# Performance work log

Hardware: AMD Instinct MI355X
Metric: run time of the kernel (lower is better)

Reference implementation:

```python
import jax, jax.numpy as jnp
import numpy as np

HIDDEN = 2048
N_HEADS = 32
N_KV_HEADS = 8
HEAD_DIM = HIDDEN // N_HEADS  # 64
N_REP = N_HEADS // N_KV_HEADS  # 4
ROPE_THETA = 10000.0


def setup_inputs() -> dict:
    key = jax.random.key(0)
    ks = jax.random.split(key, 5)
    b, s = 2, 2048
    x = jax.random.normal(ks[0], (b, s, HIDDEN), dtype=jnp.float32)
    position_ids = jnp.arange(b * s, dtype=jnp.int32).reshape(b, s)
    sc = 1.0 / np.sqrt(HIDDEN)
    Wq = jax.random.normal(ks[1], (HIDDEN, HIDDEN), dtype=jnp.float32) * sc
    Wk = jax.random.normal(ks[2], (HIDDEN, N_KV_HEADS * HEAD_DIM), dtype=jnp.float32) * sc
    Wv = jax.random.normal(ks[3], (HIDDEN, N_KV_HEADS * HEAD_DIM), dtype=jnp.float32) * sc
    Wo = jax.random.normal(ks[4], (HIDDEN, HIDDEN), dtype=jnp.float32) * sc
    return {"input_ids": x, "Wq": Wq, "Wk": Wk, "Wv": Wv, "Wo": Wo,
            "position_ids": position_ids}


def _rope_cos_sin(position_ids, dtype):
    # inv_freq: [head_dim/2]
    inv_freq = 1.0 / (ROPE_THETA ** (jnp.arange(0, HEAD_DIM, 2, dtype=jnp.float32) / HEAD_DIM))
    freqs = position_ids.astype(jnp.float32)[..., None] * inv_freq  # [b, s, d/2]
    emb = jnp.concatenate([freqs, freqs], axis=-1)  # [b, s, d]
    return emb.astype(dtype), None  # placeholder, replaced below


def _rotate_half(x):
    x1, x2 = jnp.split(x, 2, axis=-1)
    return jnp.concatenate([-x2, x1], axis=-1)


def reference(input_ids, Wq, Wk, Wv, Wo, position_ids):
    b, s, _ = input_ids.shape
    q = (input_ids @ Wq).reshape(b, s, N_HEADS, HEAD_DIM).transpose(0, 2, 1, 3)      # [b,H,s,d]
    k = (input_ids @ Wk).reshape(b, s, N_KV_HEADS, HEAD_DIM).transpose(0, 2, 1, 3)   # [b,Hkv,s,d]
    v = (input_ids @ Wv).reshape(b, s, N_KV_HEADS, HEAD_DIM).transpose(0, 2, 1, 3)

    # RoPE
    inv_freq = 1.0 / (ROPE_THETA ** (jnp.arange(0, HEAD_DIM, 2, dtype=jnp.float32) / HEAD_DIM))
    freqs = position_ids.astype(jnp.float32)[..., None] * inv_freq  # [b,s,d/2]
    emb = jnp.concatenate([freqs, freqs], axis=-1)                   # [b,s,d]
    cos = jnp.cos(emb).astype(input_ids.dtype)[:, None, :, :]        # [b,1,s,d]
    sin = jnp.sin(emb).astype(input_ids.dtype)[:, None, :, :]
    q = q * cos + _rotate_half(q) * sin
    k = k * cos + _rotate_half(k) * sin

    # repeat_kv: [b,Hkv,s,d] -> [b,H,s,d]
    k = jnp.repeat(k, N_REP, axis=1)
    v = jnp.repeat(v, N_REP, axis=1)

    # causal SDPA
    scale = 1.0 / np.sqrt(HEAD_DIM)
    scores = jnp.einsum('bhqd,bhkd->bhqk', q, k) * scale
    causal = jnp.tril(jnp.ones((s, s), dtype=bool))
    scores = jnp.where(causal, scores, jnp.finfo(scores.dtype).min)
    attn = jax.nn.softmax(scores, axis=-1)
    out = jnp.einsum('bhqk,bhkd->bhqd', attn, v)                     # [b,H,s,d]
    out = out.transpose(0, 2, 1, 3).reshape(b, s, HIDDEN)
    return out @ Wo
```

## Files before the change

### kernel.cpp

```cpp
#include <hip/hip_runtime.h>
#include <hip/hip_bf16.h>

#define HIDDEN 2048
#define NHEADS 32
#define NKVH   8
#define HD     64
#define BATCH  2
#define SEQ    2048
#define ROWS   (BATCH * SEQ)
#define NQKV   3072
#define KCOL   2048
#define VCOL   2560

typedef __bf16 bf16x8 __attribute__((ext_vector_type(8)));
typedef float  f32x4  __attribute__((ext_vector_type(4)));

__device__ __forceinline__ void gl2lds16(const void* g, void* l) {
  __builtin_amdgcn_global_load_lds(
      (const __attribute__((address_space(1))) void*)g,
      (__attribute__((address_space(3))) void*)l, 16, 0, 0);
}

__global__ void convert_bf16(const float* __restrict__ src, __bf16* __restrict__ dst,
                             int n8) {
  int i = blockIdx.x * blockDim.x + threadIdx.x;
  if (i >= n8) return;
  const float4* s = (const float4*)(src + (size_t)i * 8);
  float4 a = s[0], b = s[1];
  bf16x8 o;
  o[0] = (__bf16)a.x; o[1] = (__bf16)a.y; o[2] = (__bf16)a.z; o[3] = (__bf16)a.w;
  o[4] = (__bf16)b.x; o[5] = (__bf16)b.y; o[6] = (__bf16)b.z; o[7] = (__bf16)b.w;
  *(bf16x8*)(dst + (size_t)i * 8) = o;
}

__global__ void wtrans(const float* __restrict__ Wq, const float* __restrict__ Wk,
                       const float* __restrict__ Wv, const float* __restrict__ Wo,
                       __bf16* __restrict__ dst) {
  __shared__ __bf16 tile[32][33];
  int n0 = blockIdx.x * 32, k0 = blockIdx.y * 32;
  int tx = threadIdx.x, ty = threadIdx.y;
  const float* src;
  int N, c0;
  if (n0 < 2048)      { src = Wq; N = 2048; c0 = n0; }
  else if (n0 < 2560) { src = Wk; N = 512;  c0 = n0 - 2048; }
  else if (n0 < 3072) { src = Wv; N = 512;  c0 = n0 - 2560; }
  else                { src = Wo; N = 2048; c0 = n0 - 3072; }
#pragma unroll
  for (int i = 0; i < 32; i += 8)
    tile[ty + i][tx] = (__bf16)src[(size_t)(k0 + ty + i) * N + (c0 + tx)];
  __syncthreads();
#pragma unroll
  for (int i = 0; i < 32; i += 8)
    dst[(size_t)(n0 + ty + i) * HIDDEN + (k0 + tx)] = tile[tx][ty + i];
}

__global__ void vtrans(const __bf16* __restrict__ QKV, __bf16* __restrict__ Vt) {
  __shared__ __bf16 tile[64][65];
  int s0 = blockIdx.x * 64, bh = blockIdx.y;
  int b = bh >> 3, hk = bh & 7;
  int tx = threadIdx.x, ty = threadIdx.y;
#pragma unroll
  for (int i = 0; i < 16; ++i) {
    int r = ty * 16 + i;
    tile[r][tx] = QKV[(size_t)(b * SEQ + s0 + r) * NQKV + VCOL + hk * HD + tx];
  }
  __syncthreads();
#pragma unroll
  for (int i = 0; i < 16; ++i) {
    int d = ty * 16 + i;
    Vt[((size_t)bh * HD + d) * SEQ + s0 + tx] = tile[tx][d];
  }
}

template <typename OutT, bool ROPE>
__launch_bounds__(256, 2)
__global__ void gemm_bt(const __bf16* __restrict__ A, const __bf16* __restrict__ Bt,
                        OutT* __restrict__ C, int M, int N, int K,
                        const int* __restrict__ pos_ids) {
  __shared__ __bf16 As[128 * 32];
  __shared__ __bf16 Bs[128 * 32];
  int bn = blockIdx.x, bm = blockIdx.y;
  int t = threadIdx.x;
  int wave = t >> 6, lane = t & 63, l16 = lane & 15, quad = lane >> 4;
  int wm = (wave >> 1) * 64, wn = (wave & 1) * 64;

  f32x4 acc[4][4] = {};

  int arow = t >> 2;
  int ac   = (t & 3) * 8;
  const __bf16* Ag = A  + (size_t)(bm * 128 + arow) * K + ac;
  const __bf16* Bg = Bt + (size_t)(bn * 128 + arow) * K + ac;
  __bf16* AsW0 = As + wave * 512;
  __bf16* AsW1 = As + 2048 + wave * 512;
  __bf16* BsW0 = Bs + wave * 512;
  __bf16* BsW1 = Bs + 2048 + wave * 512;

  for (int k0 = 0; k0 < K; k0 += 32) {
    __syncthreads();
    gl2lds16(Ag + k0, AsW0);
    gl2lds16(Ag + (size_t)64 * K + k0, AsW1);
    gl2lds16(Bg + k0, BsW0);
    gl2lds16(Bg + (size_t)64 * K + k0, BsW1);
    __syncthreads();

    bf16x8 af[4], bfr[4];
#pragma unroll
    for (int i = 0; i < 4; ++i) {
      af[i]  = *(const bf16x8*)(&As[(wm + i * 16 + l16) * 32 + quad * 8]);
      bfr[i] = *(const bf16x8*)(&Bs[(wn + i * 16 + l16) * 32 + quad * 8]);
    }
#pragma unroll
    for (int i = 0; i < 4; ++i)
#pragma unroll
      for (int j = 0; j < 4; ++j)
        acc[i][j] = __builtin_amdgcn_mfma_f32_16x16x32_bf16(af[i], bfr[j], acc[i][j], 0, 0, 0);
  }

  if (ROPE) {
    int headidx = bn * 2 + (wn >> 6);
    if (headidx < 40) {
      float invrev0 = __expf(-(float)l16 * 0.28782313662425574f) * 0.15915494309189535f;
      float invrev1 = __expf(-(float)(l16 + 16) * 0.28782313662425574f) * 0.15915494309189535f;
#pragma unroll
      for (int i = 0; i < 4; ++i)
#pragma unroll
        for (int r = 0; r < 4; ++r) {
          int gr = bm * 128 + wm + i * 16 + quad * 4 + r;
          float pos = (float)pos_ids[gr];
          float rv0 = pos * invrev0; rv0 -= floorf(rv0);
          float rv1 = pos * invrev1; rv1 -= floorf(rv1);
          float a0 = rv0 * 6.283185307179586f, a1 = rv1 * 6.283185307179586f;
          float s0 = __sinf(a0), c0 = __cosf(a0);
          float s1 = __sinf(a1), c1 = __cosf(a1);
          float x0 = acc[i][0][r], x2 = acc[i][2][r];
          acc[i][0][r] = x0 * c0 - x2 * s0;
          acc[i][2][r] = x2 * c0 + x0 * s0;
          float x1 = acc[i][1][r], x3 = acc[i][3][r];
          acc[i][1][r] = x1 * c1 - x3 * s1;
          acc[i][3][r] = x3 * c1 + x1 * s1;
        }
    }
  }

#pragma unroll
  for (int i = 0; i < 4; ++i)
#pragma unroll
    for (int j = 0; j < 4; ++j)
#pragma unroll
      for (int r = 0; r < 4; ++r)
        C[(size_t)(bm * 128 + wm + i * 16 + quad * 4 + r) * N +
          (bn * 128 + wn + j * 16 + l16)] = (OutT)acc[i][j][r];
}

#define PSTRP 72
__launch_bounds__(256, 3)
__global__ void flash_attn(const __bf16* __restrict__ QKV, const __bf16* __restrict__ Vt,
                           __bf16* __restrict__ O) {
  int qt = 31 - (blockIdx.x >> 1);
  int h2 = blockIdx.x & 1;
  int hk = blockIdx.y, b = blockIdx.z;
  int t = threadIdx.x;
  int wave = t >> 6, lane = t & 63, l16 = lane & 15, quad = lane >> 4;
  int hh = h2 * 2 + (wave >> 1);
  int h  = hk * 4 + hh;
  int qs = wave & 1;

  __shared__ __bf16 Ks[2][2][64 * 32];
  __shared__ __bf16 Vs[2][2][64 * 32];
  __shared__ __bf16 Ps[4][32 * PSTRP];
  __bf16* PsW = Ps[wave];

  const __bf16* Kbase = QKV + (size_t)(b * SEQ) * NQKV + KCOL + hk * HD;
  const __bf16* VtB   = Vt + (size_t)(b * NKVH + hk) * HD * SEQ;

  int kr = wave * 16 + (lane >> 2);
  int kc = (lane & 3) * 8;
  int vd = wave * 16 + (lane >> 2);
  int vc = (lane & 3) * 8;

  bf16x8 qfrag[2][2];
#pragma unroll
  for (int qi = 0; qi < 2; ++qi) {
    const __bf16* qp = QKV + (size_t)(b * SEQ + qt * 64 + qs * 32 + qi * 16 + l16) * NQKV
                     + h * HD + quad * 8;
    bf16x8 q0 = *(const bf16x8*)qp;
    bf16x8 q1 = *(const bf16x8*)(qp + 32);
#pragma unroll
    for (int e = 0; e < 8; ++e) {
      qfrag[qi][0][e] = (__bf16)((float)q0[e] * 0.125f);
      qfrag[qi][1][e] = (__bf16)((float)q1[e] * 0.125f);
    }
  }

  float lsum[2][4];
  f32x4 oacc[2][4];
#pragma unroll
  for (int qi = 0; qi < 2; ++qi) {
#pragma unroll
    for (int r = 0; r < 4; ++r) lsum[qi][r] = 0.f;
#pragma unroll
    for (int nt = 0; nt < 4; ++nt) oacc[qi][nt] = (f32x4){0.f, 0.f, 0.f, 0.f};
  }

  {
    const __bf16* kp = Kbase + (size_t)kr * NQKV + kc;
    gl2lds16(kp,      &Ks[0][0][wave * 512]);
    gl2lds16(kp + 32, &Ks[0][1][wave * 512]);
    const __bf16* vp = VtB + (size_t)vd * SEQ + vc;
    gl2lds16(vp,      &Vs[0][0][wave * 512]);
    gl2lds16(vp + 32, &Vs[0][1][wave * 512]);
  }

  for (int kt = 0; kt <= qt; ++kt) {
    int buf = kt & 1;
    __syncthreads();
    if (kt < qt) {
      const __bf16* kp = Kbase + (size_t)((kt + 1) * 64 + kr) * NQKV + kc;
      gl2lds16(kp,      &Ks[buf ^ 1][0][wave * 512]);
      gl2lds16(kp + 32, &Ks[buf ^ 1][1][wave * 512]);
      const __bf16* vp = VtB + (size_t)vd * SEQ + (kt + 1) * 64 + vc;
      gl2lds16(vp,      &Vs[buf ^ 1][0][wave * 512]);
      gl2lds16(vp + 32, &Vs[buf ^ 1][1][wave * 512]);
    }

    f32x4 sacc[2][4];
#pragma unroll
    for (int qi = 0; qi < 2; ++qi)
#pragma unroll
      for (int nt = 0; nt < 4; ++nt) sacc[qi][nt] = (f32x4){0.f, 0.f, 0.f, 0.f};
#pragma unroll
    for (int ks = 0; ks < 2; ++ks)
#pragma unroll
      for (int nt = 0; nt < 4; ++nt) {
        bf16x8 kf = *(const bf16x8*)(&Ks[buf][ks][(nt * 16 + l16) * 32 + quad * 8]);
#pragma unroll
        for (int qi = 0; qi < 2; ++qi)
          sacc[qi][nt] = __builtin_amdgcn_mfma_f32_16x16x32_bf16(qfrag[qi][ks], kf, sacc[qi][nt], 0, 0, 0);
      }

    float pv[2][4][4];
    if (kt == qt) {
#pragma unroll
      for (int qi = 0; qi < 2; ++qi)
#pragma unroll
        for (int nt = 0; nt < 4; ++nt)
#pragma unroll
          for (int r = 0; r < 4; ++r) {
            int kg = nt * 16 + l16;
            int qg = qs * 32 + qi * 16 + quad * 4 + r;
            pv[qi][nt][r] = __expf((kg > qg) ? -1e30f : sacc[qi][nt][r]);
          }
    } else {
#pragma unroll
      for (int qi = 0; qi < 2; ++qi)
#pragma unroll
        for (int nt = 0; nt < 4; ++nt)
#pragma unroll
          for (int r = 0; r < 4; ++r)
            pv[qi][nt][r] = __expf(sacc[qi][nt][r]);
    }
#pragma unroll
    for (int qi = 0; qi < 2; ++qi)
#pragma unroll
      for (int r = 0; r < 4; ++r)
        lsum[qi][r] += (pv[qi][0][r] + pv[qi][1][r]) + (pv[qi][2][r] + pv[qi][3][r]);

#pragma unroll
    for (int qi = 0; qi < 2; ++qi)
#pragma unroll
      for (int nt = 0; nt < 4; ++nt)
#pragma unroll
        for (int r = 0; r < 4; ++r)
          PsW[(qi * 16 + quad * 4 + r) * PSTRP + nt * 16 + l16] = (__bf16)pv[qi][nt][r];

#pragma unroll
    for (int ks = 0; ks < 2; ++ks) {
      bf16x8 pf[2], vf[4];
#pragma unroll
      for (int qi = 0; qi < 2; ++qi)
        pf[qi] = *(const bf16x8*)(&PsW[(qi * 16 + l16) * PSTRP + ks * 32 + quad * 8]);
#pragma unroll
      for (int nt = 0; nt < 4; ++nt)
        vf[nt] = *(const bf16x8*)(&Vs[buf][ks][(nt * 16 + l16) * 32 + quad * 8]);
#pragma unroll
      for (int qi = 0; qi < 2; ++qi)
#pragma unroll
        for (int nt = 0; nt < 4; ++nt)
          oacc[qi][nt] = __builtin_amdgcn_mfma_f32_16x16x32_bf16(pf[qi], vf[nt], oacc[qi][nt], 0, 0, 0);
    }
  }

#pragma unroll
  for (int qi = 0; qi < 2; ++qi)
#pragma unroll
    for (int r = 0; r < 4; ++r) {
      float l = lsum[qi][r];
#pragma unroll
      for (int off = 1; off < 16; off <<= 1) l += __shfl_xor(l, off);
      float inv = 1.0f / l;
#pragma unroll
      for (int nt = 0; nt < 4; ++nt) {
        float o = oacc[qi][nt][r] * inv;
        O[(size_t)(b * SEQ + qt * 64 + qs * 32 + qi * 16 + quad * 4 + r) * HIDDEN +
          h * HD + nt * 16 + l16] = (__bf16)o;
      }
    }
}

extern "C" void kernel_launch(void* const* d_in, const int* in_sizes, int n_in,
                              void* d_out, int out_size, void* d_ws, size_t ws_size,
                              hipStream_t stream) {
  const float* x  = (const float*)d_in[0];
  const float* Wq = (const float*)d_in[1];
  const float* Wk = (const float*)d_in[2];
  const float* Wv = (const float*)d_in[3];
  const float* Wo = (const float*)d_in[4];
  const int* pos  = (const int*)d_in[5];

  __bf16* Wqkvt = (__bf16*)d_ws;
  __bf16* Wot   = Wqkvt + (size_t)NQKV * HIDDEN;
  __bf16* Xb    = Wot + (size_t)HIDDEN * HIDDEN;
  __bf16* QKV   = Xb + (size_t)ROWS * HIDDEN;
  __bf16* Oat   = QKV + (size_t)ROWS * NQKV;
  __bf16* Vt    = Xb;

  wtrans<<<dim3(160, 64), dim3(32, 8), 0, stream>>>(Wq, Wk, Wv, Wo, Wqkvt);
  convert_bf16<<<(ROWS * HIDDEN / 8 + 255) / 256, 256, 0, stream>>>(x, Xb, ROWS * HIDDEN / 8);

  gemm_bt<__bf16, true><<<dim3(NQKV / 128, ROWS / 128), 256, 0, stream>>>(
      Xb, Wqkvt, QKV, ROWS, NQKV, HIDDEN, pos);

  vtrans<<<dim3(SEQ / 64, BATCH * NKVH), dim3(64, 4), 0, stream>>>(QKV, Vt);

  flash_attn<<<dim3(64, NKVH, BATCH), 256, 0, stream>>>(QKV, Vt, Oat);

  gemm_bt<float, false><<<dim3(HIDDEN / 128, ROWS / 128), 256, 0, stream>>>(
      Oat, Wot, (float*)d_out, ROWS, HIDDEN, HIDDEN, nullptr);
}
```

Before: 324.6 us.

## Fuse V transpose into QKV GEMM, pair causal tiles, keep P in registers

The QKV GEMM epilogue now writes V straight into the transposed Vt layout, so the separate vtrans kernel is gone. Flash attention computes S transposed (K as the A operand), which lets the exponentiated probabilities feed the PV MFMA directly from registers through 16x16x16 bf16 MFMAs. This removes the LDS round trip for P. Each block handles a pair of query tiles (p and 31-p) to balance causal work across a grid half the size. The trade-offs are a V re-layout through registers into LDS and extra MFMA instructions at K=16.

Result: faster. 287.7 us (-11.4%).

```diff
diff --git a/kernel.cpp b/kernel.cpp
--- a/kernel.cpp
+++ b/kernel.cpp
@@ -13,12 +13,33 @@
 #define VCOL   2560
 
 typedef __bf16 bf16x8 __attribute__((ext_vector_type(8)));
+typedef __bf16 bf16x4 __attribute__((ext_vector_type(4)));
 typedef float  f32x4  __attribute__((ext_vector_type(4)));
+typedef short  s16x4  __attribute__((ext_vector_type(4)));
+typedef short  s16x8  __attribute__((ext_vector_type(8)));
 
 __device__ __forceinline__ void gl2lds16(const void* g, void* l) {
   __builtin_amdgcn_global_load_lds(
       (const __attribute__((address_space(1))) void*)g,
       (__attribute__((address_space(3))) void*)l, 16, 0, 0);
+}
+
+__device__ __forceinline__ short f2bs(float f) {
+  __bf16 h = (__bf16)f;
+  return __builtin_bit_cast(short, h);
+}
+
+__device__ __forceinline__ f32x4 mfma16(s16x4 a, s16x4 b, f32x4 c) {
+#if __has_builtin(__builtin_amdgcn_mfma_f32_16x16x16bf16_1k)
+  return __builtin_amdgcn_mfma_f32_16x16x16bf16_1k(a, b, c, 0, 0, 0);
+#else
+  s16x8 z = {0,0,0,0,0,0,0,0};
+  s16x8 a8 = __builtin_shufflevector(a, (s16x4){0,0,0,0}, 0,1,2,3,4,5,6,7);
+  s16x8 b8 = __builtin_shufflevector(b, (s16x4){0,0,0,0}, 0,1,2,3,4,5,6,7);
+  a8[4]=0;a8[5]=0;a8[6]=0;a8[7]=0; b8[4]=0;b8[5]=0;b8[6]=0;b8[7]=0;
+  return __builtin_amdgcn_mfma_f32_16x16x32_bf16(
+      __builtin_bit_cast(bf16x8, a8), __builtin_bit_cast(bf16x8, b8), c, 0, 0, 0);
+#endif
 }
 
 __global__ void convert_bf16(const float* __restrict__ src, __bf16* __restrict__ dst,
@@ -54,29 +75,11 @@
     dst[(size_t)(n0 + ty + i) * HIDDEN + (k0 + tx)] = tile[tx][ty + i];
 }
 
-__global__ void vtrans(const __bf16* __restrict__ QKV, __bf16* __restrict__ Vt) {
-  __shared__ __bf16 tile[64][65];
-  int s0 = blockIdx.x * 64, bh = blockIdx.y;
-  int b = bh >> 3, hk = bh & 7;
-  int tx = threadIdx.x, ty = threadIdx.y;
-#pragma unroll
-  for (int i = 0; i < 16; ++i) {
-    int r = ty * 16 + i;
-    tile[r][tx] = QKV[(size_t)(b * SEQ + s0 + r) * NQKV + VCOL + hk * HD + tx];
-  }
-  __syncthreads();
-#pragma unroll
-  for (int i = 0; i < 16; ++i) {
-    int d = ty * 16 + i;
-    Vt[((size_t)bh * HD + d) * SEQ + s0 + tx] = tile[tx][d];
-  }
-}
-
 template <typename OutT, bool ROPE>
 __launch_bounds__(256, 2)
 __global__ void gemm_bt(const __bf16* __restrict__ A, const __bf16* __restrict__ Bt,
                         OutT* __restrict__ C, int M, int N, int K,
-                        const int* __restrict__ pos_ids) {
+                        const int* __restrict__ pos_ids, __bf16* __restrict__ Vt) {
   __shared__ __bf16 As[128 * 32];
   __shared__ __bf16 Bs[128 * 32];
   int bn = blockIdx.x, bm = blockIdx.y;
@@ -118,28 +121,43 @@
 
   if (ROPE) {
     int headidx = bn * 2 + (wn >> 6);
-    if (headidx < 40) {
-      float invrev0 = __expf(-(float)l16 * 0.28782313662425574f) * 0.15915494309189535f;
-      float invrev1 = __expf(-(float)(l16 + 16) * 0.28782313662425574f) * 0.15915494309189535f;
-#pragma unroll
-      for (int i = 0; i < 4; ++i)
-#pragma unroll
-        for (int r = 0; r < 4; ++r) {
-          int gr = bm * 128 + wm + i * 16 + quad * 4 + r;
-          float pos = (float)pos_ids[gr];
-          float rv0 = pos * invrev0; rv0 -= floorf(rv0);
-          float rv1 = pos * invrev1; rv1 -= floorf(rv1);
-          float a0 = rv0 * 6.283185307179586f, a1 = rv1 * 6.283185307179586f;
-          float s0 = __sinf(a0), c0 = __cosf(a0);
-          float s1 = __sinf(a1), c1 = __cosf(a1);
-          float x0 = acc[i][0][r], x2 = acc[i][2][r];
-          acc[i][0][r] = x0 * c0 - x2 * s0;
-          acc[i][2][r] = x2 * c0 + x0 * s0;
-          float x1 = acc[i][1][r], x3 = acc[i][3][r];
-          acc[i][1][r] = x1 * c1 - x3 * s1;
-          acc[i][3][r] = x3 * c1 + x1 * s1;
+    if (headidx >= 40) {
+#pragma unroll
+      for (int i = 0; i < 4; ++i) {
+        int srow = bm * 128 + wm + i * 16 + quad * 4;
+        int b = srow >> 11, s = srow & 2047;
+#pragma unroll
+        for (int j = 0; j < 4; ++j) {
+          int vcol = bn * 128 + wn + j * 16 + l16 - VCOL;
+          int hk = vcol >> 6, d = vcol & 63;
+          bf16x4 w;
+#pragma unroll
+          for (int r = 0; r < 4; ++r) w[r] = (__bf16)acc[i][j][r];
+          *(bf16x4*)(Vt + ((size_t)(b * NKVH + hk) * HD + d) * SEQ + s) = w;
         }
-    }
+      }
+      return;
+    }
+    float invrev0 = __expf(-(float)l16 * 0.28782313662425574f) * 0.15915494309189535f;
+    float invrev1 = __expf(-(float)(l16 + 16) * 0.28782313662425574f) * 0.15915494309189535f;
+#pragma unroll
+    for (int i = 0; i < 4; ++i)
+#pragma unroll
+      for (int r = 0; r < 4; ++r) {
+        int gr = bm * 128 + wm + i * 16 + quad * 4 + r;
+        float pos = (float)pos_ids[gr];
+        float rv0 = pos * invrev0; rv0 -= floorf(rv0);
+        float rv1 = pos * invrev1; rv1 -= floorf(rv1);
+        float a0 = rv0 * 6.283185307179586f, a1 = rv1 * 6.283185307179586f;
+        float s0 = __sinf(a0), c0 = __cosf(a0);
+        float s1 = __sinf(a1), c1 = __cosf(a1);
+        float x0 = acc[i][0][r], x2 = acc[i][2][r];
+        acc[i][0][r] = x0 * c0 - x2 * s0;
+        acc[i][2][r] = x2 * c0 + x0 * s0;
+        float x1 = acc[i][1][r], x3 = acc[i][3][r];
+        acc[i][1][r] = x1 * c1 - x3 * s1;
+        acc[i][3][r] = x3 * c1 + x1 * s1;
+      }
   }
 
 #pragma unroll
@@ -152,12 +170,10 @@
           (bn * 128 + wn + j * 16 + l16)] = (OutT)acc[i][j][r];
 }
 
-#define PSTRP 72
 __launch_bounds__(256, 3)
 __global__ void flash_attn(const __bf16* __restrict__ QKV, const __bf16* __restrict__ Vt,
                            __bf16* __restrict__ O) {
-  int qt = 31 - (blockIdx.x >> 1);
-  int h2 = blockIdx.x & 1;
+  int p = blockIdx.x >> 1, h2 = blockIdx.x & 1;
   int hk = blockIdx.y, b = blockIdx.z;
   int t = threadIdx.x;
   int wave = t >> 6, lane = t & 63, l16 = lane & 15, quad = lane >> 4;
@@ -166,9 +182,7 @@
   int qs = wave & 1;
 
   __shared__ __bf16 Ks[2][2][64 * 32];
-  __shared__ __bf16 Vs[2][2][64 * 32];
-  __shared__ __bf16 Ps[4][32 * PSTRP];
-  __bf16* PsW = Ps[wave];
+  __shared__ __bf16 Vs[2][4096];
 
   const __bf16* Kbase = QKV + (size_t)(b * SEQ) * NQKV + KCOL + hk * HD;
   const __bf16* VtB   = Vt + (size_t)(b * NKVH + hk) * HD * SEQ;
@@ -176,135 +190,147 @@
   int kr = wave * 16 + (lane >> 2);
   int kc = (lane & 3) * 8;
   int vd = wave * 16 + (lane >> 2);
-  int vc = (lane & 3) * 8;
-
-  bf16x8 qfrag[2][2];
-#pragma unroll
-  for (int qi = 0; qi < 2; ++qi) {
-    const __bf16* qp = QKV + (size_t)(b * SEQ + qt * 64 + qs * 32 + qi * 16 + l16) * NQKV
-                     + h * HD + quad * 8;
-    bf16x8 q0 = *(const bf16x8*)qp;
-    bf16x8 q1 = *(const bf16x8*)(qp + 32);
-#pragma unroll
-    for (int e = 0; e < 8; ++e) {
-      qfrag[qi][0][e] = (__bf16)((float)q0[e] * 0.125f);
-      qfrag[qi][1][e] = (__bf16)((float)q1[e] * 0.125f);
+  int vsc = (lane & 3) * 16;
+  int vs4w = (lane & 3) * 4;
+
+  for (int seg = 0; seg < 2; ++seg) {
+    int qt = seg ? (31 - p) : p;
+
+    __syncthreads();
+
+    bf16x8 qfrag[2][2];
+#pragma unroll
+    for (int qi = 0; qi < 2; ++qi) {
+      const __bf16* qp = QKV + (size_t)(b * SEQ + qt * 64 + qs * 32 + qi * 16 + l16) * NQKV
+                       + h * HD + quad * 8;
+      bf16x8 q0 = *(const bf16x8*)qp;
+      bf16x8 q1 = *(const bf16x8*)(qp + 32);
+#pragma unroll
+      for (int e = 0; e < 8; ++e) {
+        qfrag[qi][0][e] = (__bf16)((float)q0[e] * 0.125f);
+        qfrag[qi][1][e] = (__bf16)((float)q1[e] * 0.125f);
+      }
+    }
+
+    float lsum[2] = {0.f, 0.f};
+    f32x4 oacc[2][4];
+#pragma unroll
+    for (int qi = 0; qi < 2; ++qi)
+#pragma unroll
+      for (int dt = 0; dt < 4; ++dt) oacc[qi][dt] = (f32x4){0.f, 0.f, 0.f, 0.f};
+
+    {
+      const __bf16* kp = Kbase + (size_t)kr * NQKV + kc;
+      gl2lds16(kp,      &Ks[0][0][wave * 512]);
+      gl2lds16(kp + 32, &Ks[0][1][wave * 512]);
+      const __bf16* vp = VtB + (size_t)vd * SEQ + vsc;
+      s16x8 v0 = __builtin_bit_cast(s16x8, *(const bf16x8*)vp);
+      s16x8 v1 = __builtin_bit_cast(s16x8, *(const bf16x8*)(vp + 8));
+      *(s16x4*)(&Vs[0][(vs4w + 0) * 256 + vd * 4]) = __builtin_shufflevector(v0, v0, 0, 1, 2, 3);
+      *(s16x4*)(&Vs[0][(vs4w + 1) * 256 + vd * 4]) = __builtin_shufflevector(v0, v0, 4, 5, 6, 7);
+      *(s16x4*)(&Vs[0][(vs4w + 2) * 256 + vd * 4]) = __builtin_shufflevector(v1, v1, 0, 1, 2, 3);
+      *(s16x4*)(&Vs[0][(vs4w + 3) * 256 + vd * 4]) = __builtin_shufflevector(v1, v1, 4, 5, 6, 7);
+    }
+
+    for (int kt = 0; kt <= qt; ++kt) {
+      int buf = kt & 1;
+      __syncthreads();
+
+      bool pre = (kt < qt);
+      s16x8 pv0, pv1;
+      if (pre) {
+        const __bf16* kp = Kbase + (size_t)((kt + 1) * 64 + kr) * NQKV + kc;
+        gl2lds16(kp,      &Ks[buf ^ 1][0][wave * 512]);
+        gl2lds16(kp + 32, &Ks[buf ^ 1][1][wave * 512]);
+        const __bf16* vp = VtB + (size_t)vd * SEQ + (kt + 1) * 64 + vsc;
+        pv0 = __builtin_bit_cast(s16x8, *(const bf16x8*)vp);
+        pv1 = __builtin_bit_cast(s16x8, *(const bf16x8*)(vp + 8));
+      }
+
+      f32x4 sacc[2][4];
+#pragma unroll
+      for (int qi = 0; qi < 2; ++qi)
+#pragma unroll
+        for (int nt = 0; nt < 4; ++nt) sacc[qi][nt] = (f32x4){0.f, 0.f, 0.f, 0.f};
+#pragma unroll
+      for (int ks = 0; ks < 2; ++ks) {
+        bf16x8 kf[4];
+#pragma unroll
+        for (int nt = 0; nt < 4; ++nt)
+          kf[nt] = *(const bf16x8*)(&Ks[buf][ks][(nt * 16 + l16) * 32 + quad * 8]);
+#pragma unroll
+        for (int nt = 0; nt < 4; ++nt)
+#pragma unroll
+          for (int qi = 0; qi < 2; ++qi)
+            sacc[qi][nt] = __builtin_amdgcn_mfma_f32_16x16x32_bf16(kf[nt], qfrag[qi][ks], sacc[qi][nt], 0, 0, 0);
+      }
+
+      s16x4 af[2][4];
+      if (kt == qt) {
+#pragma unroll
+        for (int qi = 0; qi < 2; ++qi)
+#pragma unroll
+          for (int nt = 0; nt < 4; ++nt)
+#pragma unroll
+            for (int r = 0; r < 4; ++r) {
+              int kg = nt * 16 + quad * 4 + r;
+              int qg = qs * 32 + qi * 16 + l16;
+              float e = __expf((kg > qg) ? -1e30f : sacc[qi][nt][r]);
+              lsum[qi] += e;
+              af[qi][nt][r] = f2bs(e);
+            }
+      } else {
+#pragma unroll
+        for (int qi = 0; qi < 2; ++qi)
+#pragma unroll
+          for (int nt = 0; nt < 4; ++nt)
+#pragma unroll
+            for (int r = 0; r < 4; ++r) {
+              float e = __expf(sacc[qi][nt][r]);
+              lsum[qi] += e;
+              af[qi][nt][r] = f2bs(e);
+            }
+      }
+
+#pragma unroll
+      for (int nt = 0; nt < 4; ++nt) {
+        s16x4 vf[4];
+#pragma unroll
+        for (int dt = 0; dt < 4; ++dt)
+          vf[dt] = *(const s16x4*)(&Vs[buf][(nt * 4 + quad) * 256 + (dt * 16 + l16) * 4]);
+#pragma unroll
+        for (int qi = 0; qi < 2; ++qi)
+#pragma unroll
+          for (int dt = 0; dt < 4; ++dt)
+            oacc[qi][dt] = mfma16(af[qi][nt], vf[dt], oacc[qi][dt]);
+      }
+
+      if (pre) {
+        *(s16x4*)(&Vs[buf ^ 1][(vs4w + 0) * 256 + vd * 4]) = __builtin_shufflevector(pv0, pv0, 0, 1, 2, 3);
+        *(s16x4*)(&Vs[buf ^ 1][(vs4w + 1) * 256 + vd * 4]) = __builtin_shufflevector(pv0, pv0, 4, 5, 6, 7);
+        *(s16x4*)(&Vs[buf ^ 1][(vs4w + 2) * 256 + vd * 4]) = __builtin_shufflevector(pv1, pv1, 0, 1, 2, 3);
+        *(s16x4*)(&Vs[buf ^ 1][(vs4w + 3) * 256 + vd * 4]) = __builtin_shufflevector(pv1, pv1, 4, 5, 6, 7);
+      }
+    }
+
+#pragma unroll
+    for (int qi = 0; qi < 2; ++qi) {
+      float l = lsum[qi];
+      l += __shfl_xor(l, 16);
+      l += __shfl_xor(l, 32);
+#pragma unroll
+      for (int r = 0; r < 4; ++r) {
+        float lr = __shfl(l, quad * 4 + r);
+        float inv = 1.0f / lr;
+#pragma unroll
+        for (int dt = 0; dt < 4; ++dt) {
+          float o = oacc[qi][dt][r] * inv;
+          O[(size_t)(b * SEQ + qt * 64 + qs * 32 + qi * 16 + quad * 4 + r) * HIDDEN +
+            h * HD + dt * 16 + l16] = (__bf16)o;
+        }
+      }
     }
   }
-
-  float lsum[2][4];
-  f32x4 oacc[2][4];
-#pragma unroll
-  for (int qi = 0; qi < 2; ++qi) {
-#pragma unroll
-    for (int r = 0; r < 4; ++r) lsum[qi][r] = 0.f;
-#pragma unroll
-    for (int nt = 0; nt < 4; ++nt) oacc[qi][nt] = (f32x4){0.f, 0.f, 0.f, 0.f};
-  }
-
-  {
-    const __bf16* kp = Kbase + (size_t)kr * NQKV + kc;
-    gl2lds16(kp,      &Ks[0][0][wave * 512]);
-    gl2lds16(kp + 32, &Ks[0][1][wave * 512]);
-    const __bf16* vp = VtB + (size_t)vd * SEQ + vc;
-    gl2lds16(vp,      &Vs[0][0][wave * 512]);
-    gl2lds16(vp + 32, &Vs[0][1][wave * 512]);
-  }
-
-  for (int kt = 0; kt <= qt; ++kt) {
-    int buf = kt & 1;
-    __syncthreads();
-    if (kt < qt) {
-      const __bf16* kp = Kbase + (size_t)((kt + 1) * 64 + kr) * NQKV + kc;
-      gl2lds16(kp,      &Ks[buf ^ 1][0][wave * 512]);
-      gl2lds16(kp + 32, &Ks[buf ^ 1][1][wave * 512]);
-      const __bf16* vp = VtB + (size_t)vd * SEQ + (kt + 1) * 64 + vc;
-      gl2lds16(vp,      &Vs[buf ^ 1][0][wave * 512]);
-      gl2lds16(vp + 32, &Vs[buf ^ 1][1][wave * 512]);
-    }
-
-    f32x4 sacc[2][4];
-#pragma unroll
-    for (int qi = 0; qi < 2; ++qi)
-#pragma unroll
-      for (int nt = 0; nt < 4; ++nt) sacc[qi][nt] = (f32x4){0.f, 0.f, 0.f, 0.f};
-#pragma unroll
-    for (int ks = 0; ks < 2; ++ks)
-#pragma unroll
-      for (int nt = 0; nt < 4; ++nt) {
-        bf16x8 kf = *(const bf16x8*)(&Ks[buf][ks][(nt * 16 + l16) * 32 + quad * 8]);
-#pragma unroll
-        for (int qi = 0; qi < 2; ++qi)
-          sacc[qi][nt] = __builtin_amdgcn_mfma_f32_16x16x32_bf16(qfrag[qi][ks], kf, sacc[qi][nt], 0, 0, 0);
-      }
-
-    float pv[2][4][4];
-    if (kt == qt) {
-#pragma unroll
-      for (int qi = 0; qi < 2; ++qi)
-#pragma unroll
-        for (int nt = 0; nt < 4; ++nt)
-#pragma unroll
-          for (int r = 0; r < 4; ++r) {
-            int kg = nt * 16 + l16;
-            int qg = qs * 32 + qi * 16 + quad * 4 + r;
-            pv[qi][nt][r] = __expf((kg > qg) ? -1e30f : sacc[qi][nt][r]);
-          }
-    } else {
-#pragma unroll
-      for (int qi = 0; qi < 2; ++qi)
-#pragma unroll
-        for (int nt = 0; nt < 4; ++nt)
-#pragma unroll
-          for (int r = 0; r < 4; ++r)
-            pv[qi][nt][r] = __expf(sacc[qi][nt][r]);
-    }
-#pragma unroll
-    for (int qi = 0; qi < 2; ++qi)
-#pragma unroll
-      for (int r = 0; r < 4; ++r)
-        lsum[qi][r] += (pv[qi][0][r] + pv[qi][1][r]) + (pv[qi][2][r] + pv[qi][3][r]);
-
-#pragma unroll
-    for (int qi = 0; qi < 2; ++qi)
-#pragma unroll
-      for (int nt = 0; nt < 4; ++nt)
-#pragma unroll
-        for (int r = 0; r < 4; ++r)
-          PsW[(qi * 16 + quad * 4 + r) * PSTRP + nt * 16 + l16] = (__bf16)pv[qi][nt][r];
-
-#pragma unroll
-    for (int ks = 0; ks < 2; ++ks) {
-      bf16x8 pf[2], vf[4];
-#pragma unroll
-      for (int qi = 0; qi < 2; ++qi)
-        pf[qi] = *(const bf16x8*)(&PsW[(qi * 16 + l16) * PSTRP + ks * 32 + quad * 8]);
-#pragma unroll
-      for (int nt = 0; nt < 4; ++nt)
-        vf[nt] = *(const bf16x8*)(&Vs[buf][ks][(nt * 16 + l16) * 32 + quad * 8]);
-#pragma unroll
-      for (int qi = 0; qi < 2; ++qi)
-#pragma unroll
-        for (int nt = 0; nt < 4; ++nt)
-          oacc[qi][nt] = __builtin_amdgcn_mfma_f32_16x16x32_bf16(pf[qi], vf[nt], oacc[qi][nt], 0, 0, 0);
-    }
-  }
-
-#pragma unroll
-  for (int qi = 0; qi < 2; ++qi)
-#pragma unroll
-    for (int r = 0; r < 4; ++r) {
-      float l = lsum[qi][r];
-#pragma unroll
-      for (int off = 1; off < 16; off <<= 1) l += __shfl_xor(l, off);
-      float inv = 1.0f / l;
-#pragma unroll
-      for (int nt = 0; nt < 4; ++nt) {
-        float o = oacc[qi][nt][r] * inv;
-        O[(size_t)(b * SEQ + qt * 64 + qs * 32 + qi * 16 + quad * 4 + r) * HIDDEN +
-          h * HD + nt * 16 + l16] = (__bf16)o;
-      }
-    }
 }
 
 extern "C" void kernel_launch(void* const* d_in, const int* in_sizes, int n_in,
@@ -328,12 +354,10 @@
   convert_bf16<<<(ROWS * HIDDEN / 8 + 255) / 256, 256, 0, stream>>>(x, Xb, ROWS * HIDDEN / 8);
 
   gemm_bt<__bf16, true><<<dim3(NQKV / 128, ROWS / 128), 256, 0, stream>>>(
-      Xb, Wqkvt, QKV, ROWS, NQKV, HIDDEN, pos);
-
-  vtrans<<<dim3(SEQ / 64, BATCH * NKVH), dim3(64, 4), 0, stream>>>(QKV, Vt);
-
-  flash_attn<<<dim3(64, NKVH, BATCH), 256, 0, stream>>>(QKV, Vt, Oat);
+      Xb, Wqkvt, QKV, ROWS, NQKV, HIDDEN, pos, Vt);
+
+  flash_attn<<<dim3(32, NKVH, BATCH), 256, 0, stream>>>(QKV, Vt, Oat);
 
   gemm_bt<float, false><<<dim3(HIDDEN / 128, ROWS / 128), 256, 0, stream>>>(
-      Oat, Wot, (float*)d_out, ROWS, HIDDEN, HIDDEN, nullptr);
-}
+      Oat, Wot, (float*)d_out, ROWS, HIDDEN, HIDDEN, nullptr, nullptr);
+}
```
